# Optimization experiments

Measured on AMD Instinct MI355X. Metric: run time of the kernel, lower is better.

Reference implementation:

```python
import jax, jax.numpy as jnp
import numpy as np

N, E, H, IN_FEAT, NUM_GRAPHS, NUM_CLASSES, L, HID = 50000, 600000, 128, 7, 256, 2, 5, 256
EPS_MSG = 1e-7
EPS_SOFTMAX = 1e-16
LN_EPS = 1e-5


def layer_norm(x, g, b):
    mu = jnp.mean(x, axis=-1, keepdims=True)
    var = jnp.mean((x - mu) ** 2, axis=-1, keepdims=True)
    return (x - mu) * jax.lax.rsqrt(var + LN_EPS) * g + b


def setup_inputs() -> dict:
    key = jax.random.key(0)
    ks = jax.random.split(key, 16)
    s = 0.05
    return {
        "x": jax.random.normal(ks[0], (N, IN_FEAT), jnp.float32),
        "edge_index": jax.random.randint(ks[1], (2, E), 0, N),
        "batch": jnp.sort(jax.random.randint(ks[2], (N,), 0, NUM_GRAPHS)),
        "enc_W": jax.random.normal(ks[3], (IN_FEAT, H), jnp.float32) * s,
        "enc_b": jnp.zeros((H,), jnp.float32),
        "t": jnp.ones((L,), jnp.float32),  # learn_t, init t=1.0
        "W1": jax.random.normal(ks[4], (L, H, HID), jnp.float32) * s,
        "b1": jnp.zeros((L, HID), jnp.float32),
        "g1": jnp.ones((L, HID), jnp.float32),
        "bb1": jnp.zeros((L, HID), jnp.float32),
        "W2": jax.random.normal(ks[5], (L, HID, H), jnp.float32) * s,
        "b2": jnp.zeros((L, H), jnp.float32),
        "ln_g": jnp.ones((L, H), jnp.float32),
        "ln_b": jnp.zeros((L, H), jnp.float32),
        "cls_W": jax.random.normal(ks[6], (H, NUM_CLASSES), jnp.float32) * s,
        "cls_b": jnp.zeros((NUM_CLASSES,), jnp.float32),
    }


def reference(x, edge_index, batch, enc_W, enc_b, t, W1, b1, g1, bb1, W2, b2, ln_g, ln_b, cls_W, cls_b):
    n = x.shape[0]
    src, dst = edge_index[0], edge_index[1]  # messages flow src -> dst
    h = x @ enc_W + enc_b  # node_encoder, [N, H]
    for i in range(t.shape[0]):  # DeepGCNLayer, block='res+'
        z = jax.nn.relu(layer_norm(h, ln_g[i], ln_b[i]))
        # GENConv message: relu(x_j) + eps (edge_attr is None)
        msg = jax.nn.relu(z[src]) + EPS_MSG  # [E, H]
        # scatter-softmax aggregation with temperature t
        logits = msg * t[i]
        m = jax.ops.segment_max(logits, dst, num_segments=n)  # [N, H]
        ex = jnp.exp(logits - m[dst])
        den = jax.ops.segment_sum(ex, dst, num_segments=n) + EPS_SOFTMAX
        agg = jax.ops.segment_sum(ex * msg, dst, num_segments=n) / den
        # GENConv update MLP: Linear -> LayerNorm -> ReLU -> Linear on (agg + x)
        out = agg + z
        hm = jax.nn.relu(layer_norm(out @ W1[i] + b1[i], g1[i], bb1[i]))
        h = h + (hm @ W2[i] + b2[i])  # residual
    pooled = jax.ops.segment_sum(h, batch, num_segments=NUM_GRAPHS)  # global_add_pool
    return pooled @ cls_W + cls_b
```

## Files before the change

kernel.cpp:

```cpp
#include <hip/hip_runtime.h>
#include <hip/hip_bf16.h>

#define HD 128
#define HIDD 256
#define EPS_MSG 1e-7f
#define EPS_SM 1e-16f
#define LN_EPS 1e-5f
#define HP2 264
#define LOG2E 1.44269504f

typedef __attribute__((ext_vector_type(8))) short bf16x8;
typedef __attribute__((ext_vector_type(4))) float f32x4;
typedef __attribute__((ext_vector_type(4))) ushort u16x4;

static __device__ __forceinline__ float wave_reduce_sum(float v) {
#pragma unroll
    for (int off = 32; off >= 1; off >>= 1) v += __shfl_xor(v, off, 64);
    return v;
}

static __device__ __forceinline__ float u2f(unsigned v) {
    union { float f; unsigned u; } x;
    x.u = v;
    return x.f;
}
static __device__ __forceinline__ ushort f2bf(float f) {
    __hip_bfloat16 b = __float2bfloat16(f);
    return *(ushort*)&b;
}
static __device__ __forceinline__ unsigned packbf(float lo, float hi) {
    return (unsigned)f2bf(lo) | ((unsigned)f2bf(hi) << 16);
}

__global__ __launch_bounds__(256) void enc_ln_kernel(const float* __restrict__ x,
                                                     const float* __restrict__ W,
                                                     const float* __restrict__ b,
                                                     const float* __restrict__ g,
                                                     const float* __restrict__ bt,
                                                     unsigned* __restrict__ hp,
                                                     unsigned* __restrict__ zp, int N) {
    int node = blockIdx.x * 4 + (threadIdx.x >> 6);
    int lane = threadIdx.x & 63;
    if (node >= N) return;
    float xr[7];
#pragma unroll
    for (int j = 0; j < 7; ++j) xr[j] = x[node * 7 + j];
    float v0 = b[lane], v1 = b[lane + 64];
#pragma unroll
    for (int j = 0; j < 7; ++j) {
        v0 = fmaf(xr[j], W[j * HD + lane], v0);
        v1 = fmaf(xr[j], W[j * HD + lane + 64], v1);
    }
    float s = wave_reduce_sum(v0 + v1);
    float ss = wave_reduce_sum(v0 * v0 + v1 * v1);
    float mu = s * (1.f / 128.f);
    float var = ss * (1.f / 128.f) - mu * mu;
    float rstd = rsqrtf(var + LN_EPS);
    float z0 = fmaxf((v0 - mu) * rstd * g[lane] + bt[lane], 0.f);
    float z1 = fmaxf((v1 - mu) * rstd * g[lane + 64] + bt[lane + 64], 0.f);
    int i0 = (2 * lane) & 63, i1 = (2 * lane + 1) & 63;
    float he_lo = __shfl(v0, i0), ho_lo = __shfl(v0, i1);
    float he_hi = __shfl(v1, i0), ho_hi = __shfl(v1, i1);
    float hce = (lane < 32) ? he_lo : he_hi;
    float hco = (lane < 32) ? ho_lo : ho_hi;
    hp[(size_t)node * 64 + lane] = packbf(hce, hco);
    float e_lo = __shfl(z0, i0), o_lo = __shfl(z0, i1);
    float e_hi = __shfl(z1, i0), o_hi = __shfl(z1, i1);
    float ce = (lane < 32) ? e_lo : e_hi;
    float co = (lane < 32) ? o_lo : o_hi;
    zp[(size_t)node * 64 + lane] = packbf(ce, co);
}

__global__ __launch_bounds__(256) void wconv_kernel(const float* __restrict__ W1,
                                                    const float* __restrict__ W2,
                                                    ushort* __restrict__ W1t,
                                                    ushort* __restrict__ W2t, int L) {
    int gid = blockIdx.x * 256 + threadIdx.x;
    int per = HD * HIDD;
    int tot = L * per;
    if (gid < tot) {
        int l = gid / per, r = gid % per;
        int n = r >> 7, k = r & 127;
        W1t[gid] = f2bf(W1[(size_t)l * per + (size_t)k * HIDD + n]);
    } else if (gid < 2 * tot) {
        int g2 = gid - tot;
        int l = g2 / per, r = g2 % per;
        int n = r >> 8, k = r & 255;
        W2t[g2] = f2bf(W2[(size_t)l * per + (size_t)k * HD + n]);
    }
}

__global__ __launch_bounds__(256) void count_kernel(const int* __restrict__ dst, int* __restrict__ cnt, int E) {
    int e = blockIdx.x * 256 + threadIdx.x;
    if (e < E) atomicAdd(&cnt[dst[e]], 1);
}

__global__ __launch_bounds__(256) void scanA_kernel(const int* __restrict__ cnt, int* __restrict__ row_ptr,
                                                    int* __restrict__ blk_sums, int n) {
    __shared__ int sb[256];
    int tid = threadIdx.x;
    int idx = blockIdx.x * 256 + tid;
    int v = (idx < n) ? cnt[idx] : 0;
    sb[tid] = v;
    __syncthreads();
#pragma unroll
    for (int off = 1; off < 256; off <<= 1) {
        int x = (tid >= off) ? sb[tid - off] : 0;
        __syncthreads();
        sb[tid] += x;
        __syncthreads();
    }
    if (idx < n) row_ptr[idx + 1] = sb[tid];
    if (tid == 255) blk_sums[blockIdx.x] = sb[255];
}

__global__ __launch_bounds__(256) void scanB_kernel(int* __restrict__ blk_sums, int nblk) {
    __shared__ int sb[256];
    int tid = threadIdx.x;
    int v = (tid < nblk) ? blk_sums[tid] : 0;
    sb[tid] = v;
    __syncthreads();
#pragma unroll
    for (int off = 1; off < 256; off <<= 1) {
        int x = (tid >= off) ? sb[tid - off] : 0;
        __syncthreads();
        sb[tid] += x;
        __syncthreads();
    }
    if (tid < nblk) blk_sums[tid] = sb[tid];
}

__global__ __launch_bounds__(256) void scanC_kernel(int* __restrict__ row_ptr, const int* __restrict__ blk_sums, int n) {
    int idx = blockIdx.x * 256 + threadIdx.x;
    if (idx == 0) row_ptr[0] = 0;
    if (idx < n) {
        int b = idx >> 8;
        if (b > 0) row_ptr[idx + 1] += blk_sums[b - 1];
    }
}

__global__ __launch_bounds__(256) void cursor_init_kernel(const int* __restrict__ row_ptr, int* __restrict__ cursor, int n) {
    int idx = blockIdx.x * 256 + threadIdx.x;
    if (idx < n) cursor[idx] = row_ptr[idx];
}

__global__ __launch_bounds__(256) void scatter_kernel(const int* __restrict__ src, const int* __restrict__ dst,
                                                      int* __restrict__ cursor, int* __restrict__ esrc, int E) {
    int e = blockIdx.x * 256 + threadIdx.x;
    if (e < E) {
        int v = dst[e];
        int pos = atomicAdd(&cursor[v], 1);
        esrc[pos] = src[e];
    }
}

__global__ __launch_bounds__(256) void agg_kernel(const unsigned* __restrict__ zp,
                                                  const int* __restrict__ row_ptr,
                                                  const int* __restrict__ esrc,
                                                  const float* __restrict__ t_all, int layer,
                                                  unsigned* __restrict__ obuf, int N) {
    int node = __builtin_amdgcn_readfirstlane(blockIdx.x * 4 + (threadIdx.x >> 6));
    int lane = threadIdx.x & 63;
    if (node >= N) return;
    const float tv = t_all[layer];
    const float M = 12.f * fmaxf(tv, 1.f);
    const float tv2 = tv * LOG2E;
    const float mM2 = -M * LOG2E;
    int beg = row_ptr[node], end = row_ptr[node + 1];

    float se0 = 0.f, se1 = 0.f, sw0 = 0.f, sw1 = 0.f;
    float te0 = 0.f, te1 = 0.f, tw0 = 0.f, tw1 = 0.f;

#define AGG_EDGE(P, E0, E1, W0, W1)                                   \
    {                                                                  \
        float a0 = u2f((P) << 16) + EPS_MSG;                           \
        float a1 = u2f((P) & 0xffff0000u) + EPS_MSG;                   \
        float x0 = __builtin_amdgcn_exp2f(fmaf(a0, tv2, mM2));         \
        float x1 = __builtin_amdgcn_exp2f(fmaf(a1, tv2, mM2));         \
        E0 += x0;                                                      \
        E1 += x1;                                                      \
        W0 = fmaf(x0, a0, W0);                                         \
        W1 = fmaf(x1, a1, W1);                                         \
    }

    int e = beg;
    for (; e + 4 <= end; e += 4) {
        int s0 = esrc[e], s1 = esrc[e + 1], s2 = esrc[e + 2], s3 = esrc[e + 3];
        unsigned p0 = zp[(size_t)s0 * 64 + lane];
        unsigned p1 = zp[(size_t)s1 * 64 + lane];
        unsigned p2 = zp[(size_t)s2 * 64 + lane];
        unsigned p3 = zp[(size_t)s3 * 64 + lane];
        AGG_EDGE(p0, se0, se1, sw0, sw1)
        AGG_EDGE(p1, se0, se1, sw0, sw1)
        AGG_EDGE(p2, te0, te1, tw0, tw1)
        AGG_EDGE(p3, te0, te1, tw0, tw1)
    }
    for (; e < end; ++e) {
        unsigned p0 = zp[(size_t)esrc[e] * 64 + lane];
        AGG_EDGE(p0, se0, se1, sw0, sw1)
    }
#undef AGG_EDGE
    se0 += te0; se1 += te1; sw0 += tw0; sw1 += tw1;

    float a0 = (end > beg) ? sw0 / (se0 + EPS_SM) : 0.f;
    float a1 = (end > beg) ? sw1 / (se1 + EPS_SM) : 0.f;
    unsigned ps = zp[(size_t)node * 64 + lane];
    float z0 = u2f(ps << 16), z1 = u2f(ps & 0xffff0000u);
    obuf[(size_t)node * 64 + lane] = packbf(a0 + z0, a1 + z1);
}

__global__ __launch_bounds__(256, 4) void mlp_kernel(const ushort* __restrict__ obuf,
                                                     unsigned* __restrict__ hp,
                                                     const ushort* __restrict__ W1t, const float* __restrict__ b1,
                                                     const float* __restrict__ g1, const float* __restrict__ bb1,
                                                     const ushort* __restrict__ W2t, const float* __restrict__ b2,
                                                     const float* __restrict__ gnext, const float* __restrict__ btnext,
                                                     unsigned* __restrict__ zp, int fuse,
                                                     int N) {
    __shared__ ushort s_hm[32 * HP2];
    __shared__ float s_part[32 * 8];

    int tid = threadIdx.x;
    int wid = tid >> 6, lane = tid & 63;
    int l15 = lane & 15, q = lane >> 4;
    int row0 = blockIdx.x * 32;

    uint2 hpre[2][2];
#pragma unroll
    for (int mb = 0; mb < 2; ++mb) {
        int row = row0 + mb * 16 + l15;
#pragma unroll
        for (int nb = 0; nb < 2; ++nb) {
            if (row < N)
                hpre[mb][nb] = *(const uint2*)&hp[(size_t)row * 64 + wid * 16 + nb * 8 + q * 2];
            else {
                hpre[mb][nb].x = 0u;
                hpre[mb][nb].y = 0u;
            }
        }
    }

    f32x4 acc1[2][4];
#pragma unroll
    for (int mb = 0; mb < 2; ++mb)
#pragma unroll
        for (int nb = 0; nb < 4; ++nb) acc1[mb][nb] = (f32x4)0.f;

#pragma unroll
    for (int kk = 0; kk < 4; ++kk) {
        bf16x8 bfr[2];
#pragma unroll
        for (int mb = 0; mb < 2; ++mb) {
            int row = row0 + mb * 16 + l15;
            if (row < N)
                bfr[mb] = *(const bf16x8*)(obuf + (size_t)row * HD + kk * 32 + q * 8);
            else
                bfr[mb] = (bf16x8)0;
        }
#pragma unroll
        for (int nb = 0; nb < 4; ++nb) {
            bf16x8 wfr = *(const bf16x8*)&W1t[(size_t)(wid * 64 + nb * 16 + l15) * HD + kk * 32 + q * 8];
#pragma unroll
            for (int mb = 0; mb < 2; ++mb)
                acc1[mb][nb] = __builtin_amdgcn_mfma_f32_16x16x32_bf16(wfr, bfr[mb], acc1[mb][nb], 0, 0, 0);
        }
    }

    f32x4 b1v[4];
#pragma unroll
    for (int nb = 0; nb < 4; ++nb) b1v[nb] = *(const f32x4*)&b1[wid * 64 + nb * 16 + q * 4];

#pragma unroll
    for (int mb = 0; mb < 2; ++mb) {
        float s = 0.f, ss = 0.f;
#pragma unroll
        for (int nb = 0; nb < 4; ++nb) {
#pragma unroll
            for (int rg = 0; rg < 4; ++rg) {
                float v = acc1[mb][nb][rg] + b1v[nb][rg];
                acc1[mb][nb][rg] = v;
                s += v;
                ss += v * v;
            }
        }
        s += __shfl_xor(s, 16, 64);
        s += __shfl_xor(s, 32, 64);
        ss += __shfl_xor(ss, 16, 64);
        ss += __shfl_xor(ss, 32, 64);
        if (q == 0) {
            s_part[(mb * 16 + l15) * 8 + wid * 2] = s;
            s_part[(mb * 16 + l15) * 8 + wid * 2 + 1] = ss;
        }
    }
    __syncthreads();

    f32x4 g1v[4], bbv[4];
#pragma unroll
    for (int nb = 0; nb < 4; ++nb) {
        g1v[nb] = *(const f32x4*)&g1[wid * 64 + nb * 16 + q * 4];
        bbv[nb] = *(const f32x4*)&bb1[wid * 64 + nb * 16 + q * 4];
    }
#pragma unroll
    for (int mb = 0; mb < 2; ++mb) {
        int rl = mb * 16 + l15;
        f32x4 p0 = *(const f32x4*)&s_part[rl * 8];
        f32x4 p1 = *(const f32x4*)&s_part[rl * 8 + 4];
        float S = p0.x + p0.z + p1.x + p1.z;
        float SS = p0.y + p0.w + p1.y + p1.w;
        float mu = S * (1.f / 256.f);
        float var = SS * (1.f / 256.f) - mu * mu;
        float rstd = rsqrtf(var + LN_EPS);
#pragma unroll
        for (int nb = 0; nb < 4; ++nb) {
            u16x4 pk;
#pragma unroll
            for (int rg = 0; rg < 4; ++rg) {
                float v = fmaxf((acc1[mb][nb][rg] - mu) * rstd * g1v[nb][rg] + bbv[nb][rg], 0.f);
                pk[rg] = f2bf(v);
            }
            *(u16x4*)&s_hm[rl * HP2 + wid * 64 + nb * 16 + q * 4] = pk;
        }
    }
    __syncthreads();

    f32x4 acc2[2][2];
#pragma unroll
    for (int mb = 0; mb < 2; ++mb)
#pragma unroll
        for (int nb = 0; nb < 2; ++nb) acc2[mb][nb] = (f32x4)0.f;

#pragma unroll
    for (int kk = 0; kk < 8; ++kk) {
        bf16x8 hfr[2];
#pragma unroll
        for (int mb = 0; mb < 2; ++mb)
            hfr[mb] = *(const bf16x8*)&s_hm[(mb * 16 + l15) * HP2 + kk * 32 + q * 8];
#pragma unroll
        for (int nb = 0; nb < 2; ++nb) {
            bf16x8 wfr = *(const bf16x8*)&W2t[(size_t)(wid * 32 + nb * 16 + l15) * HIDD + kk * 32 + q * 8];
#pragma unroll
            for (int mb = 0; mb < 2; ++mb)
                acc2[mb][nb] = __builtin_amdgcn_mfma_f32_16x16x32_bf16(wfr, hfr[mb], acc2[mb][nb], 0, 0, 0);
        }
    }

    f32x4 b2v[2];
#pragma unroll
    for (int nb = 0; nb < 2; ++nb) b2v[nb] = *(const f32x4*)&b2[wid * 32 + nb * 16 + q * 4];

#pragma unroll
    for (int mb = 0; mb < 2; ++mb) {
        int row = row0 + mb * 16 + l15;
        float s2 = 0.f, ss2 = 0.f;
        if (row < N) {
#pragma unroll
            for (int nb = 0; nb < 2; ++nb) {
                uint2 hv = hpre[mb][nb];
                float h0 = u2f(hv.x << 16), h1 = u2f(hv.x & 0xffff0000u);
                float h2 = u2f(hv.y << 16), h3 = u2f(hv.y & 0xffff0000u);
                f32x4 v;
                v[0] = h0 + acc2[mb][nb][0] + b2v[nb][0];
                v[1] = h1 + acc2[mb][nb][1] + b2v[nb][1];
                v[2] = h2 + acc2[mb][nb][2] + b2v[nb][2];
                v[3] = h3 + acc2[mb][nb][3] + b2v[nb][3];
                s2 += v[0] + v[1] + v[2] + v[3];
                ss2 += v[0] * v[0] + v[1] * v[1] + v[2] * v[2] + v[3] * v[3];
                uint2 pk;
                pk.x = packbf(v[0], v[1]);
                pk.y = packbf(v[2], v[3]);
                *(uint2*)&hp[(size_t)row * 64 + wid * 16 + nb * 8 + q * 2] = pk;
                acc2[mb][nb] = v;
            }
        }
        if (fuse) {
            s2 += __shfl_xor(s2, 16, 64);
            s2 += __shfl_xor(s2, 32, 64);
            ss2 += __shfl_xor(ss2, 16, 64);
            ss2 += __shfl_xor(ss2, 32, 64);
            if (q == 0) {
                s_part[(mb * 16 + l15) * 8 + wid * 2] = s2;
                s_part[(mb * 16 + l15) * 8 + wid * 2 + 1] = ss2;
            }
        }
    }

    if (fuse) {
        __syncthreads();
        f32x4 gnv[2], bnv[2];
#pragma unroll
        for (int nb = 0; nb < 2; ++nb) {
            gnv[nb] = *(const f32x4*)&gnext[wid * 32 + nb * 16 + q * 4];
            bnv[nb] = *(const f32x4*)&btnext[wid * 32 + nb * 16 + q * 4];
        }
#pragma unroll
        for (int mb = 0; mb < 2; ++mb) {
            int rl = mb * 16 + l15;
            int row = row0 + rl;
            f32x4 p0 = *(const f32x4*)&s_part[rl * 8];
            f32x4 p1 = *(const f32x4*)&s_part[rl * 8 + 4];
            float S = p0.x + p0.z + p1.x + p1.z;
            float SS = p0.y + p0.w + p1.y + p1.w;
            float mu = S * (1.f / 128.f);
            float var = SS * (1.f / 128.f) - mu * mu;
            float rstd = rsqrtf(var + LN_EPS);
            if (row < N) {
#pragma unroll
                for (int nb = 0; nb < 2; ++nb) {
                    float z0 = fmaxf((acc2[mb][nb][0] - mu) * rstd * gnv[nb][0] + bnv[nb][0], 0.f);
                    float z1 = fmaxf((acc2[mb][nb][1] - mu) * rstd * gnv[nb][1] + bnv[nb][1], 0.f);
                    float z2 = fmaxf((acc2[mb][nb][2] - mu) * rstd * gnv[nb][2] + bnv[nb][2], 0.f);
                    float z3 = fmaxf((acc2[mb][nb][3] - mu) * rstd * gnv[nb][3] + bnv[nb][3], 0.f);
                    uint2 pk;
                    pk.x = packbf(z0, z1);
                    pk.y = packbf(z2, z3);
                    *(uint2*)&zp[(size_t)row * 64 + wid * 16 + nb * 8 + q * 2] = pk;
                }
            }
        }
    }
}

__global__ __launch_bounds__(256) void pool_kernel(const unsigned* __restrict__ hp,
                                                   const int* __restrict__ batch, int N,
                                                   float* __restrict__ pooled) {
    __shared__ int sb[2];
    __shared__ float red0[256], red1[256];
    int g = blockIdx.x;
    if (threadIdx.x == 0) {
        int lo = 0, hi = N;
        while (lo < hi) { int mid = (lo + hi) >> 1; if (batch[mid] < g) lo = mid + 1; else hi = mid; }
        sb[0] = lo;
        lo = 0; hi = N;
        int gq = g + 1;
        while (lo < hi) { int mid = (lo + hi) >> 1; if (batch[mid] < gq) lo = mid + 1; else hi = mid; }
        sb[1] = lo;
    }
    __syncthreads();
    int beg = sb[0], end = sb[1];
    int c = threadIdx.x & 63, str = threadIdx.x >> 6;
    float a0 = 0.f, a1 = 0.f;
    for (int r = beg + str; r < end; r += 4) {
        unsigned p = hp[(size_t)r * 64 + c];
        a0 += u2f(p << 16);
        a1 += u2f(p & 0xffff0000u);
    }
    red0[threadIdx.x] = a0;
    red1[threadIdx.x] = a1;
    __syncthreads();
    if (str == 0) {
        float s0 = red0[c] + red0[64 + c] + red0[128 + c] + red0[192 + c];
        float s1 = red1[c] + red1[64 + c] + red1[128 + c] + red1[192 + c];
        pooled[(size_t)g * HD + 2 * c] = s0;
        pooled[(size_t)g * HD + 2 * c + 1] = s1;
    }
}

__global__ __launch_bounds__(256) void cls_kernel(const float* __restrict__ pooled,
                                                  const float* __restrict__ W,
                                                  const float* __restrict__ b,
                                                  float* __restrict__ out, int G) {
    int gid = blockIdx.x * 256 + threadIdx.x;
    if (gid >= G * 2) return;
    int g = gid >> 1, cl = gid & 1;
    float acc = b[cl];
#pragma unroll 8
    for (int k = 0; k < HD; ++k) acc += pooled[g * HD + k] * W[k * 2 + cl];
    out[gid] = acc;
}

extern "C" void kernel_launch(void* const* d_in, const int* in_sizes, int n_in,
                              void* d_out, int out_size, void* d_ws, size_t ws_size,
                              hipStream_t stream) {
    const float* x     = (const float*)d_in[0];
    const int*   eidx  = (const int*)d_in[1];
    const int*   batch = (const int*)d_in[2];
    const float* enc_W = (const float*)d_in[3];
    const float* enc_b = (const float*)d_in[4];
    const float* t_all = (const float*)d_in[5];
    const float* W1    = (const float*)d_in[6];
    const float* b1    = (const float*)d_in[7];
    const float* g1    = (const float*)d_in[8];
    const float* bb1   = (const float*)d_in[9];
    const float* W2    = (const float*)d_in[10];
    const float* b2    = (const float*)d_in[11];
    const float* ln_g  = (const float*)d_in[12];
    const float* ln_b  = (const float*)d_in[13];
    const float* cls_W = (const float*)d_in[14];
    const float* cls_b = (const float*)d_in[15];
    float* out = (float*)d_out;

    const int N = in_sizes[0] / 7;
    const int E = in_sizes[1] / 2;
    const int L = in_sizes[5];
    const int G = out_size / 2;
    const int* src = eidx;
    const int* dst = eidx + E;

    char* p = (char*)d_ws;
    auto alloc = [&](size_t bytes) {
        char* q = p;
        p += (bytes + 255) & ~(size_t)255;
        return q;
    };
    unsigned* hp     = (unsigned*)alloc((size_t)N * 64 * 4);
    unsigned* zp     = (unsigned*)alloc((size_t)N * 64 * 4);
    unsigned* obuf   = (unsigned*)alloc((size_t)N * 64 * 4);
    float*    pooled = (float*)alloc((size_t)G * HD * 4);
    int* cnt      = (int*)alloc((size_t)N * 4);
    int* row_ptr  = (int*)alloc((size_t)(N + 1) * 4);
    int* cursor   = (int*)alloc((size_t)N * 4);
    int* blk_sums = (int*)alloc(256 * 4);
    int* esrc     = (int*)alloc((size_t)E * 4);
    ushort* W1t   = (ushort*)alloc((size_t)L * HD * HIDD * 2);
    ushort* W2t   = (ushort*)alloc((size_t)L * HD * HIDD * 2);

    const int nblkN = (N + 255) / 256;
    const int nblkE = (E + 255) / 256;

    enc_ln_kernel<<<(N + 3) / 4, 256, 0, stream>>>(x, enc_W, enc_b, ln_g, ln_b, hp, zp, N);
    {
        int tot2 = 2 * L * HD * HIDD;
        wconv_kernel<<<(tot2 + 255) / 256, 256, 0, stream>>>(W1, W2, W1t, W2t, L);
    }

    hipMemsetAsync(cnt, 0, (size_t)N * 4, stream);
    count_kernel<<<nblkE, 256, 0, stream>>>(dst, cnt, E);
    scanA_kernel<<<nblkN, 256, 0, stream>>>(cnt, row_ptr, blk_sums, N);
    scanB_kernel<<<1, 256, 0, stream>>>(blk_sums, nblkN);
    scanC_kernel<<<nblkN, 256, 0, stream>>>(row_ptr, blk_sums, N);
    cursor_init_kernel<<<nblkN, 256, 0, stream>>>(row_ptr, cursor, N);
    scatter_kernel<<<nblkE, 256, 0, stream>>>(src, dst, cursor, esrc, E);

    for (int i = 0; i < L; ++i) {
        agg_kernel<<<(N + 3) / 4, 256, 0, stream>>>(zp, row_ptr, esrc, t_all, i, obuf, N);
        int fuse = (i + 1 < L) ? 1 : 0;
        const float* gn = ln_g + (size_t)(fuse ? i + 1 : i) * HD;
        const float* bn = ln_b + (size_t)(fuse ? i + 1 : i) * HD;
        mlp_kernel<<<(N + 31) / 32, 256, 0, stream>>>((const ushort*)obuf, hp,
                                                      W1t + (size_t)i * HD * HIDD, b1 + (size_t)i * HIDD,
                                                      g1 + (size_t)i * HIDD, bb1 + (size_t)i * HIDD,
                                                      W2t + (size_t)i * HD * HIDD, b2 + (size_t)i * HD,
                                                      gn, bn, zp, fuse, N);
    }

    pool_kernel<<<G, 256, 0, stream>>>(hp, batch, N, pooled);
    cls_kernel<<<(G * 2 + 255) / 256, 256, 0, stream>>>(pooled, cls_W, cls_b, out, G);
}
```

Before: 495.2 us.

## Fuse softmax aggregation into MLP kernel with ping-pong z buffers

Merges the per-layer aggregation kernel into the MLP kernel. Each 32-row block first aggregates its own nodes (one wave per 8 nodes) into shared memory, then runs the MFMA MLP reading from LDS instead of a global obuf. The z buffer is double-buffered so that one layer's neighbor gathers read the previous z while new z is written, which removes the obuf round trip and one launch per layer. The trade-off is that aggregation now runs inside a block with launch_bounds(256,4) and more LDS, so less parallelism and latency hiding is available for the irregular gathers.

```diff
diff --git a/kernel.cpp b/kernel.cpp
--- a/kernel.cpp
+++ b/kernel.cpp
@@ -7,6 +7,7 @@
 #define EPS_SM 1e-16f
 #define LN_EPS 1e-5f
 #define HP2 264
+#define OBS 68
 #define LOG2E 1.44269504f
 
 typedef __attribute__((ext_vector_type(8))) short bf16x8;
@@ -154,22 +155,46 @@
     }
 }
 
-__global__ __launch_bounds__(256) void agg_kernel(const unsigned* __restrict__ zp,
-                                                  const int* __restrict__ row_ptr,
-                                                  const int* __restrict__ esrc,
-                                                  const float* __restrict__ t_all, int layer,
-                                                  unsigned* __restrict__ obuf, int N) {
-    int node = __builtin_amdgcn_readfirstlane(blockIdx.x * 4 + (threadIdx.x >> 6));
-    int lane = threadIdx.x & 63;
-    if (node >= N) return;
-    const float tv = t_all[layer];
-    const float M = 12.f * fmaxf(tv, 1.f);
-    const float tv2 = tv * LOG2E;
-    const float mM2 = -M * LOG2E;
-    int beg = row_ptr[node], end = row_ptr[node + 1];
-
-    float se0 = 0.f, se1 = 0.f, sw0 = 0.f, sw1 = 0.f;
-    float te0 = 0.f, te1 = 0.f, tw0 = 0.f, tw1 = 0.f;
+__global__ __launch_bounds__(256, 4) void layer_kernel(const unsigned* __restrict__ zp_in,
+                                                       unsigned* __restrict__ zp_out,
+                                                       unsigned* __restrict__ hp,
+                                                       const int* __restrict__ row_ptr,
+                                                       const int* __restrict__ esrc,
+                                                       const float* __restrict__ t_all, int layer,
+                                                       const ushort* __restrict__ W1t, const float* __restrict__ b1,
+                                                       const float* __restrict__ g1, const float* __restrict__ bb1,
+                                                       const ushort* __restrict__ W2t, const float* __restrict__ b2,
+                                                       const float* __restrict__ gnext, const float* __restrict__ btnext,
+                                                       int fuse, int N) {
+    __shared__ unsigned s_ob[32 * OBS];
+    __shared__ ushort s_hm[32 * HP2];
+    __shared__ float s_part[32 * 8];
+
+    int tid = threadIdx.x;
+    int wid = tid >> 6, lane = tid & 63;
+    int l15 = lane & 15, q = lane >> 4;
+    int row0 = blockIdx.x * 32;
+
+    uint2 hpre[2][2];
+#pragma unroll
+    for (int mb = 0; mb < 2; ++mb) {
+        int row = row0 + mb * 16 + l15;
+#pragma unroll
+        for (int nb = 0; nb < 2; ++nb) {
+            if (row < N)
+                hpre[mb][nb] = *(const uint2*)&hp[(size_t)row * 64 + wid * 16 + nb * 8 + q * 2];
+            else {
+                hpre[mb][nb].x = 0u;
+                hpre[mb][nb].y = 0u;
+            }
+        }
+    }
+
+    {
+        const float tv = t_all[layer];
+        const float M = 12.f * fmaxf(tv, 1.f);
+        const float tv2 = tv * LOG2E;
+        const float mM2 = -M * LOG2E;
 
 #define AGG_EDGE(P, E0, E1, W0, W1)                                   \
     {                                                                  \
@@ -183,62 +208,39 @@
         W1 = fmaf(x1, a1, W1);                                         \
     }
 
-    int e = beg;
-    for (; e + 4 <= end; e += 4) {
-        int s0 = esrc[e], s1 = esrc[e + 1], s2 = esrc[e + 2], s3 = esrc[e + 3];
-        unsigned p0 = zp[(size_t)s0 * 64 + lane];
-        unsigned p1 = zp[(size_t)s1 * 64 + lane];
-        unsigned p2 = zp[(size_t)s2 * 64 + lane];
-        unsigned p3 = zp[(size_t)s3 * 64 + lane];
-        AGG_EDGE(p0, se0, se1, sw0, sw1)
-        AGG_EDGE(p1, se0, se1, sw0, sw1)
-        AGG_EDGE(p2, te0, te1, tw0, tw1)
-        AGG_EDGE(p3, te0, te1, tw0, tw1)
-    }
-    for (; e < end; ++e) {
-        unsigned p0 = zp[(size_t)esrc[e] * 64 + lane];
-        AGG_EDGE(p0, se0, se1, sw0, sw1)
-    }
+        for (int j = 0; j < 8; ++j) {
+            int nd = row0 + wid * 8 + j;
+            if (nd >= N) break;
+            int beg = __builtin_amdgcn_readfirstlane(row_ptr[nd]);
+            int end = __builtin_amdgcn_readfirstlane(row_ptr[nd + 1]);
+            float se0 = 0.f, se1 = 0.f, sw0 = 0.f, sw1 = 0.f;
+            float te0 = 0.f, te1 = 0.f, tw0 = 0.f, tw1 = 0.f;
+            int e = beg;
+            for (; e + 4 <= end; e += 4) {
+                int s0 = esrc[e], s1 = esrc[e + 1], s2 = esrc[e + 2], s3 = esrc[e + 3];
+                unsigned p0 = zp_in[(size_t)s0 * 64 + lane];
+                unsigned p1 = zp_in[(size_t)s1 * 64 + lane];
+                unsigned p2 = zp_in[(size_t)s2 * 64 + lane];
+                unsigned p3 = zp_in[(size_t)s3 * 64 + lane];
+                AGG_EDGE(p0, se0, se1, sw0, sw1)
+                AGG_EDGE(p1, se0, se1, sw0, sw1)
+                AGG_EDGE(p2, te0, te1, tw0, tw1)
+                AGG_EDGE(p3, te0, te1, tw0, tw1)
+            }
+            for (; e < end; ++e) {
+                unsigned p0 = zp_in[(size_t)esrc[e] * 64 + lane];
+                AGG_EDGE(p0, se0, se1, sw0, sw1)
+            }
+            se0 += te0; se1 += te1; sw0 += tw0; sw1 += tw1;
+            float a0 = (end > beg) ? sw0 / (se0 + EPS_SM) : 0.f;
+            float a1 = (end > beg) ? sw1 / (se1 + EPS_SM) : 0.f;
+            unsigned ps = zp_in[(size_t)nd * 64 + lane];
+            float z0 = u2f(ps << 16), z1 = u2f(ps & 0xffff0000u);
+            s_ob[(wid * 8 + j) * OBS + lane] = packbf(a0 + z0, a1 + z1);
+        }
 #undef AGG_EDGE
-    se0 += te0; se1 += te1; sw0 += tw0; sw1 += tw1;
-
-    float a0 = (end > beg) ? sw0 / (se0 + EPS_SM) : 0.f;
-    float a1 = (end > beg) ? sw1 / (se1 + EPS_SM) : 0.f;
-    unsigned ps = zp[(size_t)node * 64 + lane];
-    float z0 = u2f(ps << 16), z1 = u2f(ps & 0xffff0000u);
-    obuf[(size_t)node * 64 + lane] = packbf(a0 + z0, a1 + z1);
-}
-
-__global__ __launch_bounds__(256, 4) void mlp_kernel(const ushort* __restrict__ obuf,
-                                                     unsigned* __restrict__ hp,
-                                                     const ushort* __restrict__ W1t, const float* __restrict__ b1,
-                                                     const float* __restrict__ g1, const float* __restrict__ bb1,
-                                                     const ushort* __restrict__ W2t, const float* __restrict__ b2,
-                                                     const float* __restrict__ gnext, const float* __restrict__ btnext,
-                                                     unsigned* __restrict__ zp, int fuse,
-                                                     int N) {
-    __shared__ ushort s_hm[32 * HP2];
-    __shared__ float s_part[32 * 8];
-
-    int tid = threadIdx.x;
-    int wid = tid >> 6, lane = tid & 63;
-    int l15 = lane & 15, q = lane >> 4;
-    int row0 = blockIdx.x * 32;
-
-    uint2 hpre[2][2];
-#pragma unroll
-    for (int mb = 0; mb < 2; ++mb) {
-        int row = row0 + mb * 16 + l15;
-#pragma unroll
-        for (int nb = 0; nb < 2; ++nb) {
-            if (row < N)
-                hpre[mb][nb] = *(const uint2*)&hp[(size_t)row * 64 + wid * 16 + nb * 8 + q * 2];
-            else {
-                hpre[mb][nb].x = 0u;
-                hpre[mb][nb].y = 0u;
-            }
-        }
-    }
+    }
+    __syncthreads();
 
     f32x4 acc1[2][4];
 #pragma unroll
@@ -250,13 +252,8 @@
     for (int kk = 0; kk < 4; ++kk) {
         bf16x8 bfr[2];
 #pragma unroll
-        for (int mb = 0; mb < 2; ++mb) {
-            int row = row0 + mb * 16 + l15;
-            if (row < N)
-                bfr[mb] = *(const bf16x8*)(obuf + (size_t)row * HD + kk * 32 + q * 8);
-            else
-                bfr[mb] = (bf16x8)0;
-        }
+        for (int mb = 0; mb < 2; ++mb)
+            bfr[mb] = *(const bf16x8*)&s_ob[(mb * 16 + l15) * OBS + kk * 16 + q * 4];
 #pragma unroll
         for (int nb = 0; nb < 4; ++nb) {
             bf16x8 wfr = *(const bf16x8*)&W1t[(size_t)(wid * 64 + nb * 16 + l15) * HD + kk * 32 + q * 8];
@@ -413,7 +410,7 @@
                     uint2 pk;
                     pk.x = packbf(z0, z1);
                     pk.y = packbf(z2, z3);
-                    *(uint2*)&zp[(size_t)row * 64 + wid * 16 + nb * 8 + q * 2] = pk;
+                    *(uint2*)&zp_out[(size_t)row * 64 + wid * 16 + nb * 8 + q * 2] = pk;
                 }
             }
         }
@@ -503,8 +500,8 @@
         return q;
     };
     unsigned* hp     = (unsigned*)alloc((size_t)N * 64 * 4);
-    unsigned* zp     = (unsigned*)alloc((size_t)N * 64 * 4);
-    unsigned* obuf   = (unsigned*)alloc((size_t)N * 64 * 4);
+    unsigned* zp0    = (unsigned*)alloc((size_t)N * 64 * 4);
+    unsigned* zp1    = (unsigned*)alloc((size_t)N * 64 * 4);
     float*    pooled = (float*)alloc((size_t)G * HD * 4);
     int* cnt      = (int*)alloc((size_t)N * 4);
     int* row_ptr  = (int*)alloc((size_t)(N + 1) * 4);
@@ -514,10 +511,12 @@
     ushort* W1t   = (ushort*)alloc((size_t)L * HD * HIDD * 2);
     ushort* W2t   = (ushort*)alloc((size_t)L * HD * HIDD * 2);
 
+    unsigned* zpbuf[2] = {zp0, zp1};
+
     const int nblkN = (N + 255) / 256;
     const int nblkE = (E + 255) / 256;
 
-    enc_ln_kernel<<<(N + 3) / 4, 256, 0, stream>>>(x, enc_W, enc_b, ln_g, ln_b, hp, zp, N);
+    enc_ln_kernel<<<(N + 3) / 4, 256, 0, stream>>>(x, enc_W, enc_b, ln_g, ln_b, hp, zp0, N);
     {
         int tot2 = 2 * L * HD * HIDD;
         wconv_kernel<<<(tot2 + 255) / 256, 256, 0, stream>>>(W1, W2, W1t, W2t, L);
@@ -532,15 +531,15 @@
     scatter_kernel<<<nblkE, 256, 0, stream>>>(src, dst, cursor, esrc, E);
 
     for (int i = 0; i < L; ++i) {
-        agg_kernel<<<(N + 3) / 4, 256, 0, stream>>>(zp, row_ptr, esrc, t_all, i, obuf, N);
         int fuse = (i + 1 < L) ? 1 : 0;
         const float* gn = ln_g + (size_t)(fuse ? i + 1 : i) * HD;
         const float* bn = ln_b + (size_t)(fuse ? i + 1 : i) * HD;
-        mlp_kernel<<<(N + 31) / 32, 256, 0, stream>>>((const ushort*)obuf, hp,
-                                                      W1t + (size_t)i * HD * HIDD, b1 + (size_t)i * HIDD,
-                                                      g1 + (size_t)i * HIDD, bb1 + (size_t)i * HIDD,
-                                                      W2t + (size_t)i * HD * HIDD, b2 + (size_t)i * HD,
-                                                      gn, bn, zp, fuse, N);
+        layer_kernel<<<(N + 31) / 32, 256, 0, stream>>>(zpbuf[i & 1], zpbuf[(i + 1) & 1], hp,
+                                                        row_ptr, esrc, t_all, i,
+                                                        W1t + (size_t)i * HD * HIDD, b1 + (size_t)i * HIDD,
+                                                        g1 + (size_t)i * HIDD, bb1 + (size_t)i * HIDD,
+                                                        W2t + (size_t)i * HD * HIDD, b2 + (size_t)i * HD,
+                                                        gn, bn, fuse, N);
     }
 
     pool_kernel<<<G, 256, 0, stream>>>(hp, batch, N, pooled);
```

Result: slower. 544.0 us (+9.8%).
